# Kernel tuning notes

Hardware: AMD Instinct MI355X
Metric: run time of the kernel (lower is better)

Reference implementation:

```python
import jax, jax.numpy as jnp
import numpy as np

TM, TK = 64, 64
M, K = 4096, 4096
N_BLOCKS = 1024
T_SHAPE = (1, 2048, K)


def _gelu_tanh(x):
    # Matches the Triton kernel's tanh-approx GELU:
    inner = 0.7978845608 * (x + 0.044715 * x * x * x)
    return x * 0.5 * (1.0 + jnp.tanh(inner))


def setup_inputs() -> dict:
    key = jax.random.key(0)
    k1, k2, k3, k4, k5 = jax.random.split(key, 5)
    x = jax.random.normal(k1, T_SHAPE, dtype=jnp.float32)
    values = jax.random.normal(k2, (N_BLOCKS, TM, TK), dtype=jnp.float32) * 0.02
    bias = jax.random.normal(k3, (M,), dtype=jnp.float32) * 0.02
    block_rows = jax.random.randint(k4, (N_BLOCKS,), 0, M // TM, dtype=jnp.int32)
    block_cols = jax.random.randint(k5, (N_BLOCKS,), 0, K // TK, dtype=jnp.int32)
    return {"x": x, "values": values, "bias": bias,
            "block_rows": block_rows, "block_cols": block_cols}


def reference(x, values, bias, block_rows, block_cols):
    # y = gelu(W_sparse @ x^T + bias[:, None])^T, W stored as 64x64 blocks.
    in_features = x.shape[-1]
    out_features = bias.shape[0]
    n_row_blocks = out_features // TM
    x_flat = x.reshape(-1, in_features)          # [T, K]
    T = x_flat.shape[0]
    xb = x_flat.reshape(T, in_features // TK, TK)  # [T, nKblk, TK]
    g = xb[:, block_cols, :]                     # [T, nb, TK] gather per block col
    # per-block small GEMM: values[n] @ g[t, n]^T -> [nb, T, TM]
    partial = jnp.einsum('nmk,tnk->ntm', values, g)
    # scatter-add block contributions into their output row blocks
    outb = jax.ops.segment_sum(partial, block_rows, num_segments=n_row_blocks)
    y = outb.transpose(1, 0, 2).reshape(T, out_features)  # [T, M]
    y = _gelu_tanh(y + bias[None, :])
    return y.reshape(x.shape[:-1] + (out_features,))
```

## Files before the change

kernel.cpp:

```cpp
#include <hip/hip_runtime.h>
#include <hip/hip_bf16.h>

#define K_DIM 4096
#define M_DIM 4096
#define T_DIM 2048
#define NB    1024

typedef __attribute__((ext_vector_type(8))) short bf16x8;
typedef __attribute__((ext_vector_type(4))) float f32x4;

__device__ __forceinline__ unsigned short f2bf(float f) {
    unsigned int u = __builtin_bit_cast(unsigned int, f);
    unsigned int r = (u + 0x7FFFu + ((u >> 16) & 1u)) >> 16;
    return (unsigned short)r;
}

__device__ __forceinline__ void gld16(const void* g, void* l) {
    __builtin_amdgcn_global_load_lds(
        (const __attribute__((address_space(1))) unsigned int*)g,
        (__attribute__((address_space(3))) unsigned int*)l, 16, 0, 0);
}

__global__ __launch_bounds__(256) void cvt_bf16_kernel(
    const float* __restrict__ in, uint4* __restrict__ outp, int n8)
{
    int i = blockIdx.x * 256 + threadIdx.x;
    if (i >= n8) return;
    const float4* p = (const float4*)in + 2 * (size_t)i;
    float4 a = p[0];
    float4 b = p[1];
    uint4 w;
    w.x = (unsigned)f2bf(a.x) | ((unsigned)f2bf(a.y) << 16);
    w.y = (unsigned)f2bf(a.z) | ((unsigned)f2bf(a.w) << 16);
    w.z = (unsigned)f2bf(b.x) | ((unsigned)f2bf(b.y) << 16);
    w.w = (unsigned)f2bf(b.z) | ((unsigned)f2bf(b.w) << 16);
    outp[i] = w;
}

__global__ __launch_bounds__(256, 2) void fsl_mfma_bf16_kernel(
    const unsigned short* __restrict__ xb, const unsigned short* __restrict__ vb,
    const float* __restrict__ bias, const int* __restrict__ brows,
    const int* __restrict__ bcols, float* __restrict__ out)
{
    __shared__ __align__(16) unsigned char sA[2][64 * 128];
    __shared__ __align__(16) unsigned char sB[2][64 * 128];
    __shared__ unsigned int s_list[NB];
    __shared__ int s_cnt;

    const int tid  = threadIdx.x;
    const int b    = blockIdx.x;
    const int xcd  = b & 7;
    const int slot = b >> 3;
    const int t0   = (xcd + 8 * (slot & 3)) * 64;
    const int r    = slot >> 2;

    if (tid == 0) s_cnt = 0;
    __syncthreads();
    for (int n = tid; n < NB; n += 256) {
        if (brows[n] == r) {
            int p = atomicAdd(&s_cnt, 1);
            s_list[p] = (unsigned)n | ((unsigned)bcols[n] << 16);
        }
    }
    __syncthreads();
    const int cnt = s_cnt;

    const int wave = tid >> 6;
    const int lane = tid & 63;
    const int wt   = wave >> 1;
    const int wm   = wave & 1;
    const int lrow = lane & 15;
    const int lk8  = (lane >> 4) * 8;

    f32x4 acc[2][2] = {};

    const int srr    = lane >> 3;
    const int scol16 = lane & 7;

    auto stage = [&](int i, int buf) {
        const unsigned int pc = s_list[i];
        const int n = pc & 0xFFFF;
        const int c = pc >> 16;
#pragma unroll
        for (int ch = 0; ch < 2; ++ch) {
            const int rbase = wave * 16 + ch * 8;
            const int row   = rbase + srr;
            const int sc    = (scol16 ^ (row & 7)) * 8;
            gld16(xb + (size_t)(t0 + row) * K_DIM + c * 64 + sc,
                  &sA[buf][rbase * 128]);
            gld16(vb + (size_t)n * 4096 + row * 64 + sc,
                  &sB[buf][rbase * 128]);
        }
    };

    auto compute = [&](int buf) {
#pragma unroll
        for (int ks = 0; ks < 2; ++ks) {
            bf16x8 a[2], bfr[2];
#pragma unroll
            for (int f = 0; f < 2; ++f) {
                const int trow = wt * 32 + f * 16 + lrow;
                int abyte = trow * 128 + (ks * 32 + lk8) * 2;
                abyte ^= (trow & 7) << 4;
                a[f] = *(const bf16x8*)(&sA[buf][abyte]);
                const int mrow = wm * 32 + f * 16 + lrow;
                int bbyte = mrow * 128 + (ks * 32 + lk8) * 2;
                bbyte ^= (mrow & 7) << 4;
                bfr[f] = *(const bf16x8*)(&sB[buf][bbyte]);
            }
#pragma unroll
            for (int ft = 0; ft < 2; ++ft)
#pragma unroll
                for (int fm = 0; fm < 2; ++fm)
                    acc[ft][fm] = __builtin_amdgcn_mfma_f32_16x16x32_bf16(
                        a[ft], bfr[fm], acc[ft][fm], 0, 0, 0);
        }
    };

    if (cnt > 0) stage(0, 0);
    __syncthreads();
    for (int i = 0; i < cnt; ++i) {
        if (i + 1 < cnt) stage(i + 1, (i + 1) & 1);
        compute(i & 1);
        __syncthreads();
    }

    const int mcol  = lane & 15;
    const int trow4 = (lane >> 4) * 4;
#pragma unroll
    for (int ft = 0; ft < 2; ++ft) {
#pragma unroll
        for (int fm = 0; fm < 2; ++fm) {
            const int mg = r * 64 + wm * 32 + fm * 16 + mcol;
            const float bv = bias[mg];
#pragma unroll
            for (int reg = 0; reg < 4; ++reg) {
                const int t = t0 + wt * 32 + ft * 16 + trow4 + reg;
                float v = acc[ft][fm][reg] + bv;
                float inner = 0.7978845608f * (v + 0.044715f * v * v * v);
                inner = fminf(fmaxf(inner, -15.0f), 15.0f);
                const float e  = __expf(2.0f * inner);
                const float th = 1.0f - 2.0f / (e + 1.0f);
                out[(size_t)t * M_DIM + mg] = v * 0.5f * (1.0f + th);
            }
        }
    }
}

__global__ __launch_bounds__(256, 2) void fsl_mfma_fallback(
    const float* __restrict__ x, const float* __restrict__ values,
    const float* __restrict__ bias, const int* __restrict__ brows,
    const int* __restrict__ bcols, float* __restrict__ out)
{
    __shared__ __align__(16) unsigned char sA[2][64 * 128];
    __shared__ __align__(16) unsigned char sB[2][64 * 128];
    __shared__ int s_list[NB];
    __shared__ int s_cnt;

    const int tid = threadIdx.x;
    const int r   = blockIdx.x >> 5;
    const int t0  = (blockIdx.x & 31) * 64;

    if (tid == 0) s_cnt = 0;
    __syncthreads();
    for (int n = tid; n < NB; n += 256) {
        if (brows[n] == r) {
            int p = atomicAdd(&s_cnt, 1);
            s_list[p] = n;
        }
    }
    __syncthreads();
    const int cnt = s_cnt;

    const int wave = tid >> 6;
    const int lane = tid & 63;
    const int wt   = wave >> 1;
    const int wm   = wave & 1;
    const int lrow = lane & 15;
    const int lk8  = (lane >> 4) * 8;
    const int srow = tid >> 4;
    const int scol = tid & 15;

    f32x4 acc[2][2] = {};
    float4 ra[4], rb[4];

    auto stage_load = [&](int i) {
        const int n = s_list[i];
        const int c = bcols[n];
        const float* xp = x + (size_t)(t0 + srow) * K_DIM + c * 64 + scol * 4;
        const float* vp = values + (size_t)n * 4096 + srow * 64 + scol * 4;
#pragma unroll
        for (int j = 0; j < 4; ++j) {
            ra[j] = *(const float4*)(xp + (size_t)(j * 16) * K_DIM);
            rb[j] = *(const float4*)(vp + j * 16 * 64);
        }
    };
    auto stage_write = [&](int buf) {
#pragma unroll
        for (int j = 0; j < 4; ++j) {
            const int row = srow + j * 16;
            int byte = row * 128 + scol * 8;
            byte ^= (row & 7) << 4;
            uint2 pa, pb;
            pa.x = (unsigned)f2bf(ra[j].x) | ((unsigned)f2bf(ra[j].y) << 16);
            pa.y = (unsigned)f2bf(ra[j].z) | ((unsigned)f2bf(ra[j].w) << 16);
            pb.x = (unsigned)f2bf(rb[j].x) | ((unsigned)f2bf(rb[j].y) << 16);
            pb.y = (unsigned)f2bf(rb[j].z) | ((unsigned)f2bf(rb[j].w) << 16);
            *(uint2*)(&sA[buf][byte]) = pa;
            *(uint2*)(&sB[buf][byte]) = pb;
        }
    };
    auto compute = [&](int buf) {
#pragma unroll
        for (int ks = 0; ks < 2; ++ks) {
            bf16x8 a[2], bb[2];
#pragma unroll
            for (int f = 0; f < 2; ++f) {
                const int trow = wt * 32 + f * 16 + lrow;
                int abyte = trow * 128 + (ks * 32 + lk8) * 2;
                abyte ^= (trow & 7) << 4;
                a[f] = *(const bf16x8*)(&sA[buf][abyte]);
                const int mrow = wm * 32 + f * 16 + lrow;
                int bbyte = mrow * 128 + (ks * 32 + lk8) * 2;
                bbyte ^= (mrow & 7) << 4;
                bb[f] = *(const bf16x8*)(&sB[buf][bbyte]);
            }
#pragma unroll
            for (int ft = 0; ft < 2; ++ft)
#pragma unroll
                for (int fm = 0; fm < 2; ++fm)
                    acc[ft][fm] = __builtin_amdgcn_mfma_f32_16x16x32_bf16(
                        a[ft], bb[fm], acc[ft][fm], 0, 0, 0);
        }
    };

    if (cnt > 0) { stage_load(0); stage_write(0); }
    for (int i = 0; i < cnt; ++i) {
        __syncthreads();
        const bool more = (i + 1 < cnt);
        if (more) stage_load(i + 1);
        compute(i & 1);
        if (more) stage_write((i + 1) & 1);
    }

    const int mcol  = lane & 15;
    const int trow4 = (lane >> 4) * 4;
#pragma unroll
    for (int ft = 0; ft < 2; ++ft) {
#pragma unroll
        for (int fm = 0; fm < 2; ++fm) {
            const int mg = r * 64 + wm * 32 + fm * 16 + mcol;
            const float bv = bias[mg];
#pragma unroll
            for (int reg = 0; reg < 4; ++reg) {
                const int t = t0 + wt * 32 + ft * 16 + trow4 + reg;
                float v = acc[ft][fm][reg] + bv;
                float inner = 0.7978845608f * (v + 0.044715f * v * v * v);
                inner = fminf(fmaxf(inner, -15.0f), 15.0f);
                const float e  = __expf(2.0f * inner);
                const float th = 1.0f - 2.0f / (e + 1.0f);
                out[(size_t)t * M_DIM + mg] = v * 0.5f * (1.0f + th);
            }
        }
    }
}

extern "C" void kernel_launch(void* const* d_in, const int* in_sizes, int n_in,
                              void* d_out, int out_size, void* d_ws, size_t ws_size,
                              hipStream_t stream) {
    const float* x      = (const float*)d_in[0];
    const float* values = (const float*)d_in[1];
    const float* bias   = (const float*)d_in[2];
    const int*   brows  = (const int*)d_in[3];
    const int*   bcols  = (const int*)d_in[4];
    float* out = (float*)d_out;

    const size_t x_elems = (size_t)T_DIM * K_DIM;
    const size_t v_elems = (size_t)NB * 64 * 64;
    const size_t ws_need = (x_elems + v_elems) * 2;

    if (ws_size >= ws_need) {
        unsigned short* xb = (unsigned short*)d_ws;
        unsigned short* vb = xb + x_elems;
        const int n8x = (int)(x_elems / 8);
        const int n8v = (int)(v_elems / 8);
        cvt_bf16_kernel<<<(n8x + 255) / 256, 256, 0, stream>>>(x, (uint4*)xb, n8x);
        cvt_bf16_kernel<<<(n8v + 255) / 256, 256, 0, stream>>>(values, (uint4*)vb, n8v);
        fsl_mfma_bf16_kernel<<<dim3(64 * 32), 256, 0, stream>>>(
            xb, vb, bias, brows, bcols, out);
    } else {
        fsl_mfma_fallback<<<dim3(64 * 32), 256, 0, stream>>>(
            x, values, bias, brows, bcols, out);
    }
}
```

Before: 142.8 us.

## Use 128-token tiles, blocked x layout, register-held weights and a fused prep kernel

```diff
diff --git a/kernel.cpp b/kernel.cpp
--- a/kernel.cpp
+++ b/kernel.cpp
@@ -5,6 +5,7 @@
 #define M_DIM 4096
 #define T_DIM 2048
 #define NB    1024
+#define BT    128
 
 typedef __attribute__((ext_vector_type(8))) short bf16x8;
 typedef __attribute__((ext_vector_type(4))) float f32x4;
@@ -21,38 +22,55 @@
         (__attribute__((address_space(3))) unsigned int*)l, 16, 0, 0);
 }
 
-__global__ __launch_bounds__(256) void cvt_bf16_kernel(
-    const float* __restrict__ in, uint4* __restrict__ outp, int n8)
+#define XCHUNKS (T_DIM * K_DIM / 8)
+#define VCHUNKS (NB * 64 * 64 / 8)
+__global__ __launch_bounds__(256) void prep_kernel(
+    const float* __restrict__ x, const float* __restrict__ values,
+    unsigned short* __restrict__ xb2, unsigned short* __restrict__ vb)
 {
-    int i = blockIdx.x * 256 + threadIdx.x;
-    if (i >= n8) return;
-    const float4* p = (const float4*)in + 2 * (size_t)i;
-    float4 a = p[0];
-    float4 b = p[1];
-    uint4 w;
-    w.x = (unsigned)f2bf(a.x) | ((unsigned)f2bf(a.y) << 16);
-    w.y = (unsigned)f2bf(a.z) | ((unsigned)f2bf(a.w) << 16);
-    w.z = (unsigned)f2bf(b.x) | ((unsigned)f2bf(b.y) << 16);
-    w.w = (unsigned)f2bf(b.z) | ((unsigned)f2bf(b.w) << 16);
-    outp[i] = w;
-}
-
-__global__ __launch_bounds__(256, 2) void fsl_mfma_bf16_kernel(
-    const unsigned short* __restrict__ xb, const unsigned short* __restrict__ vb,
+    const int id = blockIdx.x * 256 + threadIdx.x;
+    if (id < XCHUNKS) {
+        const int t   = id >> 9;
+        const int rem = id & 511;
+        const int c   = rem >> 3;
+        const int o   = rem & 7;
+        const float4* p = (const float4*)(x + (size_t)t * K_DIM + c * 64 + o * 8);
+        const float4 a = p[0], b = p[1];
+        uint4 w;
+        w.x = (unsigned)f2bf(a.x) | ((unsigned)f2bf(a.y) << 16);
+        w.y = (unsigned)f2bf(a.z) | ((unsigned)f2bf(a.w) << 16);
+        w.z = (unsigned)f2bf(b.x) | ((unsigned)f2bf(b.y) << 16);
+        w.w = (unsigned)f2bf(b.z) | ((unsigned)f2bf(b.w) << 16);
+        *(uint4*)(xb2 + ((size_t)c * T_DIM + t) * 64 + o * 8) = w;
+    } else if (id < XCHUNKS + VCHUNKS) {
+        const int i = id - XCHUNKS;
+        const float4* p = (const float4*)(values + (size_t)i * 8);
+        const float4 a = p[0], b = p[1];
+        uint4 w;
+        w.x = (unsigned)f2bf(a.x) | ((unsigned)f2bf(a.y) << 16);
+        w.y = (unsigned)f2bf(a.z) | ((unsigned)f2bf(a.w) << 16);
+        w.z = (unsigned)f2bf(b.x) | ((unsigned)f2bf(b.y) << 16);
+        w.w = (unsigned)f2bf(b.z) | ((unsigned)f2bf(b.w) << 16);
+        *(uint4*)(vb + (size_t)i * 8) = w;
+    }
+}
+
+__global__ __launch_bounds__(256, 4) void fsl_main(
+    const unsigned short* __restrict__ xb2, const unsigned short* __restrict__ vb,
     const float* __restrict__ bias, const int* __restrict__ brows,
     const int* __restrict__ bcols, float* __restrict__ out)
 {
-    __shared__ __align__(16) unsigned char sA[2][64 * 128];
-    __shared__ __align__(16) unsigned char sB[2][64 * 128];
+    __shared__ __align__(16) unsigned char sA[2][BT * 128];
     __shared__ unsigned int s_list[NB];
     __shared__ int s_cnt;
 
     const int tid  = threadIdx.x;
     const int b    = blockIdx.x;
-    const int xcd  = b & 7;
-    const int slot = b >> 3;
-    const int t0   = (xcd + 8 * (slot & 3)) * 64;
-    const int r    = slot >> 2;
+    const int xcd   = b & 7;
+    const int slot  = b >> 3;
+    const int ttile = xcd * 2 + (slot & 1);
+    const int t0    = ttile * BT;
+    const int r     = slot >> 1;
 
     if (tid == 0) s_cnt = 0;
     __syncthreads();
@@ -67,82 +85,96 @@
 
     const int wave = tid >> 6;
     const int lane = tid & 63;
-    const int wt   = wave >> 1;
-    const int wm   = wave & 1;
     const int lrow = lane & 15;
-    const int lk8  = (lane >> 4) * 8;
-
-    f32x4 acc[2][2] = {};
+    const int lk16 = lane >> 4;
+
+    f32x4 acc[8] = {};
 
     const int srr    = lane >> 3;
     const int scol16 = lane & 7;
 
-    auto stage = [&](int i, int buf) {
-        const unsigned int pc = s_list[i];
-        const int n = pc & 0xFFFF;
-        const int c = pc >> 16;
-#pragma unroll
-        for (int ch = 0; ch < 2; ++ch) {
-            const int rbase = wave * 16 + ch * 8;
+    auto stageA = [&](int i, int buf) {
+        const int c = (int)(s_list[i] >> 16);
+        const unsigned short* src = xb2 + ((size_t)c * T_DIM + t0) * 64;
+#pragma unroll
+        for (int ch = 0; ch < 4; ++ch) {
+            const int rbase = wave * 32 + ch * 8;
             const int row   = rbase + srr;
             const int sc    = (scol16 ^ (row & 7)) * 8;
-            gld16(xb + (size_t)(t0 + row) * K_DIM + c * 64 + sc,
-                  &sA[buf][rbase * 128]);
-            gld16(vb + (size_t)n * 4096 + row * 64 + sc,
-                  &sB[buf][rbase * 128]);
-        }
-    };
-
-    auto compute = [&](int buf) {
+            gld16(src + (size_t)row * 64 + sc, &sA[buf][rbase * 128]);
+        }
+    };
+
+    auto loadB = [&](int i, bf16x8& b0, bf16x8& b1) {
+        const int n = (int)(s_list[i] & 0xFFFF);
+        const unsigned short* vp =
+            vb + (size_t)n * 4096 + (wave * 16 + lrow) * 64 + lk16 * 8;
+        b0 = *(const bf16x8*)(vp);
+        b1 = *(const bf16x8*)(vp + 32);
+    };
+
+    auto compute = [&](int buf, bf16x8 b0, bf16x8 b1) {
 #pragma unroll
         for (int ks = 0; ks < 2; ++ks) {
-            bf16x8 a[2], bfr[2];
-#pragma unroll
-            for (int f = 0; f < 2; ++f) {
-                const int trow = wt * 32 + f * 16 + lrow;
-                int abyte = trow * 128 + (ks * 32 + lk8) * 2;
+            bf16x8 afr[8];
+#pragma unroll
+            for (int tf = 0; tf < 8; ++tf) {
+                const int trow = tf * 16 + lrow;
+                int abyte = trow * 128 + (ks * 32 + lk16 * 8) * 2;
                 abyte ^= (trow & 7) << 4;
-                a[f] = *(const bf16x8*)(&sA[buf][abyte]);
-                const int mrow = wm * 32 + f * 16 + lrow;
-                int bbyte = mrow * 128 + (ks * 32 + lk8) * 2;
-                bbyte ^= (mrow & 7) << 4;
-                bfr[f] = *(const bf16x8*)(&sB[buf][bbyte]);
-            }
-#pragma unroll
-            for (int ft = 0; ft < 2; ++ft)
-#pragma unroll
-                for (int fm = 0; fm < 2; ++fm)
-                    acc[ft][fm] = __builtin_amdgcn_mfma_f32_16x16x32_bf16(
-                        a[ft], bfr[fm], acc[ft][fm], 0, 0, 0);
-        }
-    };
-
-    if (cnt > 0) stage(0, 0);
-    __syncthreads();
-    for (int i = 0; i < cnt; ++i) {
-        if (i + 1 < cnt) stage(i + 1, (i + 1) & 1);
-        compute(i & 1);
-        __syncthreads();
-    }
-
-    const int mcol  = lane & 15;
-    const int trow4 = (lane >> 4) * 4;
-#pragma unroll
-    for (int ft = 0; ft < 2; ++ft) {
-#pragma unroll
-        for (int fm = 0; fm < 2; ++fm) {
-            const int mg = r * 64 + wm * 32 + fm * 16 + mcol;
-            const float bv = bias[mg];
-#pragma unroll
-            for (int reg = 0; reg < 4; ++reg) {
-                const int t = t0 + wt * 32 + ft * 16 + trow4 + reg;
-                float v = acc[ft][fm][reg] + bv;
-                float inner = 0.7978845608f * (v + 0.044715f * v * v * v);
-                inner = fminf(fmaxf(inner, -15.0f), 15.0f);
-                const float e  = __expf(2.0f * inner);
-                const float th = 1.0f - 2.0f / (e + 1.0f);
-                out[(size_t)t * M_DIM + mg] = v * 0.5f * (1.0f + th);
-            }
+                afr[tf] = *(const bf16x8*)(&sA[buf][abyte]);
+            }
+            const bf16x8 bb = ks ? b1 : b0;
+#pragma unroll
+            for (int tf = 0; tf < 8; ++tf)
+                acc[tf] = __builtin_amdgcn_mfma_f32_16x16x32_bf16(
+                    afr[tf], bb, acc[tf], 0, 0, 0);
+        }
+    };
+
+    bf16x8 b0e, b1e, b0o, b1o;
+    if (cnt > 0) { stageA(0, 0); loadB(0, b0e, b1e); }
+    for (int i = 0; i < cnt; i += 2) {
+        {
+            if (i + 1 < cnt) {
+                stageA(i + 1, 1);
+                loadB(i + 1, b0o, b1o);
+                asm volatile("s_waitcnt vmcnt(6)" ::: "memory");
+            } else {
+                asm volatile("s_waitcnt vmcnt(0)" ::: "memory");
+            }
+            __builtin_amdgcn_s_barrier();
+            compute(0, b0e, b1e);
+            __builtin_amdgcn_s_barrier();
+        }
+        if (i + 1 < cnt) {
+            if (i + 2 < cnt) {
+                stageA(i + 2, 0);
+                loadB(i + 2, b0e, b1e);
+                asm volatile("s_waitcnt vmcnt(6)" ::: "memory");
+            } else {
+                asm volatile("s_waitcnt vmcnt(0)" ::: "memory");
+            }
+            __builtin_amdgcn_s_barrier();
+            compute(1, b0o, b1o);
+            __builtin_amdgcn_s_barrier();
+        }
+    }
+
+    const int mg = r * 64 + wave * 16 + (lane & 15);
+    const float bv = bias[mg];
+    const int tbase = t0 + (lane >> 4) * 4;
+#pragma unroll
+    for (int tf = 0; tf < 8; ++tf) {
+#pragma unroll
+        for (int reg = 0; reg < 4; ++reg) {
+            const int t = tbase + tf * 16 + reg;
+            float v = acc[tf][reg] + bv;
+            float inner = 0.7978845608f * (v + 0.044715f * v * v * v);
+            inner = fminf(fmaxf(inner, -15.0f), 15.0f);
+            const float e  = __expf(2.0f * inner);
+            const float th = 1.0f - 2.0f / (e + 1.0f);
+            out[(size_t)t * M_DIM + mg] = v * 0.5f * (1.0f + th);
         }
     }
 }
@@ -280,14 +312,10 @@
     const size_t ws_need = (x_elems + v_elems) * 2;
 
     if (ws_size >= ws_need) {
-        unsigned short* xb = (unsigned short*)d_ws;
-        unsigned short* vb = xb + x_elems;
-        const int n8x = (int)(x_elems / 8);
-        const int n8v = (int)(v_elems / 8);
-        cvt_bf16_kernel<<<(n8x + 255) / 256, 256, 0, stream>>>(x, (uint4*)xb, n8x);
-        cvt_bf16_kernel<<<(n8v + 255) / 256, 256, 0, stream>>>(values, (uint4*)vb, n8v);
-        fsl_mfma_bf16_kernel<<<dim3(64 * 32), 256, 0, stream>>>(
-            xb, vb, bias, brows, bcols, out);
+        unsigned short* xb2 = (unsigned short*)d_ws;
+        unsigned short* vb  = xb2 + x_elems;
+        prep_kernel<<<(XCHUNKS + VCHUNKS) / 256, 256, 0, stream>>>(x, values, xb2, vb);
+        fsl_main<<<dim3(1024), 256, 0, stream>>>(xb2, vb, bias, brows, bcols, out);
     } else {
         fsl_mfma_fallback<<<dim3(64 * 32), 256, 0, stream>>>(
             x, values, bias, brows, bcols, out);
```

Result: no change. 140.5 us (-1.6%).
